# Optimization experiments

Hardware: AMD Instinct MI355X
Metric: run time of the kernel (lower is better)

Reference implementation:

```python
import jax, jax.numpy as jnp
import numpy as np

# Model hyperparameters (match init_kwargs)
J, L, A, A_PRIME = 5, 4, 4, 1
M = N = 128
C = 1
NB = 2
DELTA_J, DELTA_L = J, L
MASK_ANGLES = 4
SHIFT_R = 4  # radius (pixels) of directional correlation shifts
EPS = 1e-6


def _pair_indices():
    """Static (i1, i2) indices into the flattened [C*J*L*A] coefficient axis
    for cross-scale/angle correlation pairs: j1 <= j2 <= j1+delta_j,
    circular |l1-l2| <= delta_l, a1 in [0,A), a2 in [0,A_prime)."""
    i1, i2 = [], []
    flat = lambda c, j, l, a: ((c * J + j) * L + l) * A + a
    for c in range(C):
        for j1 in range(J):
            for j2 in range(j1, min(j1 + DELTA_J, J - 1) + 1):
                for l1 in range(L):
                    for l2 in range(L):
                        dl = min((l1 - l2) % L, (l2 - l1) % L)
                        if dl > DELTA_L:
                            continue
                        for a1 in range(A):
                            for a2 in range(A_PRIME):
                                i1.append(flat(c, j1, l1, a1))
                                i2.append(flat(c, j2, l2, a2))
    return np.asarray(i1, np.int32), np.asarray(i2, np.int32)


def _shifts():
    """Zero shift plus MASK_ANGLES directional shifts at radius SHIFT_R."""
    sh = [(0, 0)]
    for s in range(MASK_ANGLES):
        th = np.pi * s / MASK_ANGLES
        sh.append((int(round(SHIFT_R * np.cos(th))), int(round(SHIFT_R * np.sin(th)))))
    return sh


def _highpass_filters():
    """Angular-sector highpass masks in Fourier space: |k| > pi/2 split into
    MASK_ANGLES orientation sectors (angle folded to [0, pi))."""
    kx = 2 * np.pi * np.fft.fftfreq(M)[:, None]
    ky = 2 * np.pi * np.fft.fftfreq(N)[None, :]
    r = np.sqrt(kx ** 2 + ky ** 2)
    th = np.mod(np.arctan2(ky, kx), np.pi)
    h = []
    for s in range(MASK_ANGLES):
        lo, hi = np.pi * s / MASK_ANGLES, np.pi * (s + 1) / MASK_ANGLES
        h.append(((r > np.pi / 2) & (th >= lo) & (th < hi)).astype(np.float32))
    return np.stack(h)  # [MASK_ANGLES, M, N]


def setup_inputs() -> dict:
    key = jax.random.key(0)
    k = jax.random.split(key, 5)
    return {
        "x": jax.random.normal(k[0], (NB, C, M, N), jnp.float32),
        "hatpsi_re": jax.random.normal(k[1], (C, J, L, A, M, N), jnp.float32),
        "hatpsi_im": jax.random.normal(k[2], (C, J, L, A, M, N), jnp.float32),
        "hatphi_re": jax.random.normal(k[3], (M, N), jnp.float32),
        "hatphi_im": jax.random.normal(k[4], (M, N), jnp.float32),
    }


def reference(x, hatpsi_re, hatpsi_im, hatphi_re, hatphi_im):
    nb = x.shape[0]
    # --- WaveConvLayer: FFT wavelet convolution ---
    hatx = jnp.fft.fft2(x)  # [nb, C, M, N] complex
    hatpsi = hatpsi_re + 1j * hatpsi_im  # [C, J, L, A, M, N]
    xpsi = jnp.fft.ifft2(hatx[:, :, None, None, None] * hatpsi[None])  # [nb,C,J,L,A,M,N]
    # --- ReluCenterLayer: ReLU of real part, spatially centered, L2-normalized ---
    y = jax.nn.relu(xpsi.real)
    y = y - y.mean((-2, -1), keepdims=True)
    y = y / (jnp.sqrt((y * y).mean((-2, -1), keepdims=True)) + EPS)
    yf = y.reshape(nb, C * J * L * A, M, N)
    # --- CorrLayer: shifted cross-correlations over pair list ---
    i1, i2 = _pair_indices()
    a1 = yf[:, i1].reshape(nb, -1, M * N)  # [nb, P, M*N]
    a2 = yf[:, i2]                          # [nb, P, M, N]
    corrs = []
    for (dx, dy) in _shifts():  # small fixed set of shifts
        a2r = jnp.roll(a2, (dx, dy), axis=(-2, -1)).reshape(nb, -1, M * N)
        corrs.append(jnp.einsum('npx,npx->np', a1, a2r) / (M * N))
    xcorr = jnp.concatenate(corrs, axis=1)  # [nb, P * n_shifts]
    # --- LowpassLayer: phi-filtered moments (mean, mean-square) ---
    hatphi = hatphi_re + 1j * hatphi_im
    xlow_map = jnp.fft.ifft2(hatx * hatphi).real  # [nb, C, M, N]
    xlow = jnp.stack([xlow_map.mean((-2, -1)), (xlow_map ** 2).mean((-2, -1))], axis=-1)  # [nb,C,2]
    # --- HighpassLayer: per-sector highpass energy (Parseval) ---
    hhigh = jnp.asarray(_highpass_filters())  # [MASK_ANGLES, M, N]
    xhigh = (jnp.abs(hatx[:, :, None] * hhigh) ** 2).mean((-2, -1)) / (M * N)  # [nb,C,MASK_ANGLES]
    return jnp.concatenate([xcorr, xlow.reshape(nb, -1), xhigh.reshape(nb, -1)], axis=1)
```

## Files before the change

### kernel.cpp

```cpp
#include <hip/hip_runtime.h>
#include <math.h>

#define NB 2
#define NMAPS 81
#define NPSI 80
#define PIXELS 16384
#define OUT_STRIDE 4806

constexpr double PI_D = 3.14159265358979323846;

__device__ inline float2 cmulf(float2 a, float2 b) {
  return make_float2(a.x * b.x - a.y * b.y, a.x * b.y + a.y * b.x);
}

template <int CTRL>
__device__ inline float dppf(float v) {
  return __int_as_float(
      __builtin_amdgcn_update_dpp(0, __float_as_int(v), CTRL, 0xf, 0xf, true));
}

__device__ inline float shx(float v, const int mask) {
  if (mask == 1) return dppf<0xB1>(v);
  if (mask == 2) return dppf<0x4E>(v);
  if (mask == 8) return dppf<0x128>(v);
  if (mask == 32) {
    auto r = __builtin_amdgcn_permlane32_swap(__float_as_uint(v),
                                              __float_as_uint(v), false, false);
    return __uint_as_float((threadIdx.x & 32) ? r[0] : r[1]);
  }
  return __shfl_xor(v, mask);
}

__device__ inline float wred64(float v) {
  int x;
  x = __builtin_amdgcn_update_dpp(0, __float_as_int(v), 0x111, 0xf, 0xf, true); v += __int_as_float(x);
  x = __builtin_amdgcn_update_dpp(0, __float_as_int(v), 0x112, 0xf, 0xf, true); v += __int_as_float(x);
  x = __builtin_amdgcn_update_dpp(0, __float_as_int(v), 0x114, 0xf, 0xf, true); v += __int_as_float(x);
  x = __builtin_amdgcn_update_dpp(0, __float_as_int(v), 0x118, 0xf, 0xf, true); v += __int_as_float(x);
  x = __builtin_amdgcn_update_dpp(0, __float_as_int(v), 0x142, 0xa, 0xf, true); v += __int_as_float(x);
  x = __builtin_amdgcn_update_dpp(0, __float_as_int(v), 0x143, 0xc, 0xf, true); v += __int_as_float(x);
  return __int_as_float(__builtin_amdgcn_readlane(__float_as_int(v), 63));
}


__global__ __launch_bounds__(128) void k_fft_rows(const float* __restrict__ x,
                                                  float2* __restrict__ tx,
                                                  int* __restrict__ sector) {
  const int tid = threadIdx.x;
  const int blkid = blockIdx.x;
  if (blkid >= NB * 128) {
    int idx = (blkid - NB * 128) * 128 + tid;
    int i = idx >> 7, j = idx & 127;
    double fx = (double)(i < 64 ? i : i - 128) / 128.0;
    double fy = (double)(j < 64 ? j : j - 128) / 128.0;
    double kx = (2.0 * PI_D) * fx;
    double ky = (2.0 * PI_D) * fy;
    double r2 = kx * kx + ky * ky;
    const double h = PI_D / 2.0;
    int s = -1;
    if (r2 > h * h) {
      double th = atan2(ky, kx);
      th = fmod(th, PI_D);
      if (th < 0.0) th += PI_D;
      if (th < PI_D * 0.25) s = 0;
      else if (th < PI_D * 0.5) s = 1;
      else if (th < PI_D * 0.75) s = 2;
      else if (th < PI_D) s = 3;
    }
    sector[idx] = s;
    return;
  }
  __shared__ float row[128];
  __shared__ float2 wt[128];
  const int m = blkid & 127;
  const int b = blkid >> 7;
  {
    double ang = -(2.0 * PI_D / 128.0) * (double)tid;
    wt[tid] = make_float2((float)cos(ang), (float)sin(ang));
  }
  row[tid] = x[(b << 14) + (m << 7) + tid];
  __syncthreads();
  float ar = 0.f, ai = 0.f;
  int idx = 0;
  const int v = tid;
#pragma unroll 8
  for (int n = 0; n < 128; ++n) {
    float xv = row[n];
    float2 w = wt[idx];
    ar = fmaf(xv, w.x, ar);
    ai = fmaf(xv, w.y, ai);
    idx = (idx + v) & 127;
  }
  tx[(b << 14) + (m << 7) + tid] = make_float2(ar, ai);
}

__global__ __launch_bounds__(128) void k_fft_cols(const float2* __restrict__ tx,
                                                  float2* __restrict__ hatx) {
  __shared__ float2 col[128];
  __shared__ float2 wt[128];
  const int tid = threadIdx.x;
  const int v = blockIdx.x & 127;
  const int b = blockIdx.x >> 7;
  {
    double ang = -(2.0 * PI_D / 128.0) * (double)tid;
    wt[tid] = make_float2((float)cos(ang), (float)sin(ang));
  }
  col[tid] = tx[(b << 14) + (tid << 7) + v];
  __syncthreads();
  float ar = 0.f, ai = 0.f;
  int idx = 0;
  const int u = tid;
#pragma unroll 8
  for (int mm = 0; mm < 128; ++mm) {
    float2 z = col[mm];
    float2 w = wt[idx];
    ar += z.x * w.x - z.y * w.y;
    ai += z.x * w.y + z.y * w.x;
    idx = (idx + u) & 127;
  }
  hatx[(b << 14) + (tid << 7) + v] = make_float2(ar, ai);
}


#define BFLY(z)                                     \
  {                                                 \
    float tx_ = shx((z).x, mask);                   \
    float ty_ = shx((z).y, mask);                   \
    float ax_ = fmaf(s, (z).x, tx_);                \
    float ay_ = fmaf(s, (z).y, ty_);                \
    (z).x = ax_ * we.x - ay_ * we.y;                \
    (z).y = ax_ * we.y + ay_ * we.x;                \
  }

__device__ inline void fft128_inv(float2& z0, float2& z1, float2& z2, float2& z3,
                                  const float2* __restrict__ wt, int l) {
  {
    float2 w = wt[l];
    float2 a0 = make_float2(z0.x + z1.x, z0.y + z1.y);
    float2 d0 = make_float2(z0.x - z1.x, z0.y - z1.y);
    z0 = a0;
    z1 = cmulf(d0, w);
    float2 a1 = make_float2(z2.x + z3.x, z2.y + z3.y);
    float2 d1 = make_float2(z2.x - z3.x, z2.y - z3.y);
    z2 = a1;
    z3 = cmulf(d1, w);
  }
#pragma unroll
  for (int mask = 32; mask >= 1; mask >>= 1) {
    float2 w = wt[(l & (mask - 1)) * (64 / mask)];
    const bool up = (l & mask) != 0;
    const float s = up ? -1.f : 1.f;
    const float2 we = up ? w : make_float2(1.f, 0.f);
    BFLY(z0);
    BFLY(z1);
    BFLY(z2);
    BFLY(z3);
  }
}


__global__ __launch_bounds__(1024) void k_ifft2d(
    const float2* __restrict__ hatx,
    const float* __restrict__ psi_re, const float* __restrict__ psi_im,
    const float* __restrict__ phi_re, const float* __restrict__ phi_im,
    float* __restrict__ y, float2* __restrict__ meaninv,
    float* __restrict__ out) {
  __shared__ float2 Tsh[128 * 129];
  __shared__ float2 wt[64];
  __shared__ float2 red16[16];
  const int tid = threadIdx.x;
  const int l = tid & 63;
  const int w = tid >> 6;
  const int mf = blockIdx.x;
  const int b = mf / NMAPS;
  const int f = mf - b * NMAPS;
  if (tid < 64) {
    double ang = (2.0 * PI_D / 128.0) * (double)tid;
    wt[tid] = make_float2((float)cos(ang), (float)sin(ang));
  }
  __syncthreads();
  for (int r = 0; r < 4; ++r) {
    const int uA = r * 32 + (w << 1);
    const int uB = uA + 1;
    const float2* hA = hatx + (b << 14) + (uA << 7);
    float2 hA0 = hA[l], hA1 = hA[l + 64];
    float2 hB0 = hA[128 + l], hB1 = hA[128 + l + 64];
    float2 fA0, fA1, fB0, fB1;
    if (f < NPSI) {
      const int po = (f << 14) + (uA << 7);
      fA0 = make_float2(psi_re[po + l], psi_im[po + l]);
      fA1 = make_float2(psi_re[po + l + 64], psi_im[po + l + 64]);
      fB0 = make_float2(psi_re[po + 128 + l], psi_im[po + 128 + l]);
      fB1 = make_float2(psi_re[po + 128 + l + 64], psi_im[po + 128 + l + 64]);
    } else {
      const int po = (uA << 7);
      fA0 = make_float2(phi_re[po + l], phi_im[po + l]);
      fA1 = make_float2(phi_re[po + l + 64], phi_im[po + l + 64]);
      fB0 = make_float2(phi_re[po + 128 + l], phi_im[po + 128 + l]);
      fB1 = make_float2(phi_re[po + 128 + l + 64], phi_im[po + 128 + l + 64]);
    }
    float2 zA0 = cmulf(hA0, fA0), zA1 = cmulf(hA1, fA1);
    float2 zB0 = cmulf(hB0, fB0), zB1 = cmulf(hB1, fB1);
    fft128_inv(zA0, zA1, zB0, zB1, wt, l);
    Tsh[l * 129 + uA] = zA0;
    Tsh[(l + 64) * 129 + uA] = zA1;
    Tsh[l * 129 + uB] = zB0;
    Tsh[(l + 64) * 129 + uB] = zB1;
  }
  __syncthreads();
  float s1 = 0.f, s2 = 0.f;
  float* yb = y + ((size_t)(b * NPSI + f) << 14);
  const int m2 = __brev(l) >> 26;
  for (int r = 0; r < 4; ++r) {
    const int qA = r * 32 + (w << 1);
    const int qB = qA + 1;
    float2 zA0 = Tsh[qA * 129 + l], zA1 = Tsh[qA * 129 + l + 64];
    float2 zB0 = Tsh[qB * 129 + l], zB1 = Tsh[qB * 129 + l + 64];
    fft128_inv(zA0, zA1, zB0, zB1, wt, l);
    const float sc = 1.f / 16384.f;
    float rA0 = zA0.x * sc, rA1 = zA1.x * sc;
    float rB0 = zB0.x * sc, rB1 = zB1.x * sc;
    if (f < NPSI) {
      rA0 = fmaxf(rA0, 0.f); rA1 = fmaxf(rA1, 0.f);
      rB0 = fmaxf(rB0, 0.f); rB1 = fmaxf(rB1, 0.f);
      const int nA = __brev(qA) >> 25;
      const int nB = __brev(qB) >> 25;
      *(float2*)(yb + (nA << 7) + (m2 << 1)) = make_float2(rA0, rA1);
      *(float2*)(yb + (nB << 7) + (m2 << 1)) = make_float2(rB0, rB1);
    }
    s1 += rA0 + rA1 + rB0 + rB1;
    s2 += rA0 * rA0 + rA1 * rA1 + rB0 * rB0 + rB1 * rB1;
  }
  float t1 = wred64(s1), t2 = wred64(s2);
  if (l == 0) red16[w] = make_float2(t1, t2);
  __syncthreads();
  if (w == 0) {
    float2 p = (l < 16) ? red16[l] : make_float2(0.f, 0.f);
    float S1 = wred64(p.x), S2 = wred64(p.y);
    if (l == 0) {
      float mean = S1 * (1.f / 16384.f);
      float msq  = S2 * (1.f / 16384.f);
      if (f < NPSI) {
        float var = fmaxf(msq - mean * mean, 0.f);
        meaninv[b * NPSI + f] = make_float2(mean, 1.f / (sqrtf(var) + 1e-6f));
      } else {
        out[b * OUT_STRIDE + 4800] = mean;
        out[b * OUT_STRIDE + 4801] = msq;
      }
    }
  }
}

__global__ __launch_bounds__(256) void k_corrtail(
    const float* __restrict__ y, const float2* __restrict__ meaninv,
    const float2* __restrict__ hatx, const int* __restrict__ sector,
    float* __restrict__ out) {
  const int tid = threadIdx.x;
  const int l = tid & 63;
  const int w = tid >> 6;
  const int work = ((blockIdx.x & 7) * 61) + (blockIdx.x >> 3);
  if (work >= NB * 240) {
    const int b = work - NB * 240;
    if (b >= NB) return;
    __shared__ float red[4][4];
    float a0 = 0, a1 = 0, a2 = 0, a3 = 0;
    for (int k = tid; k < PIXELS; k += 256) {
      float2 hx = hatx[(b << 14) + k];
      float mag = hx.x * hx.x + hx.y * hx.y;
      int s = sector[k];
      if (s == 0) a0 += mag;
      else if (s == 1) a1 += mag;
      else if (s == 2) a2 += mag;
      else if (s == 3) a3 += mag;
    }
    a0 = wred64(a0); a1 = wred64(a1); a2 = wred64(a2); a3 = wred64(a3);
    if (l == 0) { red[w][0] = a0; red[w][1] = a1; red[w][2] = a2; red[w][3] = a3; }
    __syncthreads();
    if (tid < 4) {
      float tot = red[0][tid] + red[1][tid] + red[2][tid] + red[3][tid];
      out[b * OUT_STRIDE + 4802 + tid] = tot * (1.f / (16384.f * 16384.f));
    }
    return;
  }
  __shared__ float s2m[128 * 132];
  __shared__ float redb[4 * 20];
  __shared__ float2 mi[5];
  const int b = work / 240;
  const int r_ = work - b * 240;
  const int jj = r_ >> 4;
  const int l1 = (r_ >> 2) & 3;
  const int l2 = r_ & 3;
  int j1 = 0, rem = jj;
  while (rem >= 5 - j1) { rem -= (5 - j1); ++j1; }
  const int j2 = j1 + rem;
  const int i1b = j1 * 16 + l1 * 4;
  const int i2 = j2 * 16 + l2 * 4;
  if (tid < 4) mi[tid] = meaninv[b * NPSI + i1b + tid];
  else if (tid == 4) mi[4] = meaninv[b * NPSI + i2];
  const float* __restrict__ y1 = y + ((size_t)(b * NPSI + i1b) << 14);
  const float* __restrict__ y2 = y + ((size_t)(b * NPSI + i2) << 14);
  const int r0 = tid >> 5;
  const int c4 = (tid & 31) << 2;
#pragma unroll
  for (int k = 0; k < 16; ++k) {
    int row = k * 8 + r0;
    *(float4*)&s2m[row * 132 + c4] = *(const float4*)&y2[(row << 7) + c4];
  }
  __syncthreads();
  if (tid < 128) {
    *(float4*)&s2m[tid * 132 + 128] = *(const float4*)&s2m[tid * 132];
  }
  __syncthreads();
  const int bm4 = (c4 + 124) & 127;
  float acc[20];
#pragma unroll
  for (int o = 0; o < 20; ++o) acc[o] = 0.f;
#pragma unroll 4
  for (int k = 0; k < 16; ++k) {
    const int r = k * 8 + r0;
    const int rm0 = r * 132;
    const int rm3 = ((r + 125) & 127) * 132;
    const int rm4 = ((r + 124) & 127) * 132;
    float4 q0 = *(const float4*)&s2m[rm0 + c4];
    float4 q1 = *(const float4*)&s2m[rm0 + bm4];
    float4 q3 = *(const float4*)&s2m[rm4 + c4];
    float4 qa = *(const float4*)&s2m[rm3 + bm4];
    float4 qb = *(const float4*)&s2m[rm3 + bm4 + 4];
    float4 qd = *(const float4*)&s2m[rm3 + c4 + 4];
    const float u2x = qa.y, u2y = qa.z, u2z = qa.w, u2w = qb.x;
    const float u4x = qb.w, u4y = qd.x, u4z = qd.y, u4w = qd.z;
#pragma unroll
    for (int m = 0; m < 4; ++m) {
      float4 v = *(const float4*)&y1[(m << 14) + (r << 7) + c4];
      acc[m*5+0] = fmaf(v.w,q0.w,fmaf(v.z,q0.z,fmaf(v.y,q0.y,fmaf(v.x,q0.x,acc[m*5+0]))));
      acc[m*5+1] = fmaf(v.w,q1.w,fmaf(v.z,q1.z,fmaf(v.y,q1.y,fmaf(v.x,q1.x,acc[m*5+1]))));
      acc[m*5+2] = fmaf(v.w,u2w,fmaf(v.z,u2z,fmaf(v.y,u2y,fmaf(v.x,u2x,acc[m*5+2]))));
      acc[m*5+3] = fmaf(v.w,q3.w,fmaf(v.z,q3.z,fmaf(v.y,q3.y,fmaf(v.x,q3.x,acc[m*5+3]))));
      acc[m*5+4] = fmaf(v.w,u4w,fmaf(v.z,u4z,fmaf(v.y,u4y,fmaf(v.x,u4x,acc[m*5+4]))));
    }
  }
#pragma unroll
  for (int o = 0; o < 20; ++o) {
    float tot = wred64(acc[o]);
    if (l == 0) redb[w * 20 + o] = tot;
  }
  __syncthreads();
  if (tid < 20) {
    int m = tid / 5, s = tid - m * 5;
    float tot = redb[tid] + redb[20 + tid] + redb[40 + tid] + redb[60 + tid];
    float2 m1 = mi[m], m2 = mi[4];
    float c = m1.y * m2.y * (tot * (1.f / 16384.f) - m1.x * m2.x);
    int p = jj * 64 + l1 * 16 + l2 * 4 + m;
    out[b * OUT_STRIDE + s * 960 + p] = c;
  }
}

extern "C" void kernel_launch(void* const* d_in, const int* in_sizes, int n_in,
                              void* d_out, int out_size, void* d_ws, size_t ws_size,
                              hipStream_t stream) {
  (void)in_sizes; (void)n_in; (void)out_size; (void)ws_size;
  const float* x      = (const float*)d_in[0];
  const float* psi_re = (const float*)d_in[1];
  const float* psi_im = (const float*)d_in[2];
  const float* phi_re = (const float*)d_in[3];
  const float* phi_im = (const float*)d_in[4];
  float* out = (float*)d_out;
  char* ws = (char*)d_ws;

  constexpr size_t TX_BYTES   = (size_t)NB * PIXELS * sizeof(float2);
  constexpr size_t HATX_OFF   = TX_BYTES;
  constexpr size_t HATX_BYTES = (size_t)NB * PIXELS * sizeof(float2);
  constexpr size_t Y_OFF      = HATX_OFF + HATX_BYTES;
  constexpr size_t Y_BYTES    = (size_t)NB * NPSI * PIXELS * sizeof(float);
  constexpr size_t MI_OFF     = Y_OFF + Y_BYTES;
  constexpr size_t MI_BYTES   = (size_t)NB * NPSI * sizeof(float2);
  constexpr size_t SEC_OFF    = MI_OFF + MI_BYTES;

  float2* tx       = (float2*)(ws);
  float2* hatx     = (float2*)(ws + HATX_OFF);
  float*  y        = (float*)(ws + Y_OFF);
  float2* meaninv  = (float2*)(ws + MI_OFF);
  int*    sector   = (int*)(ws + SEC_OFF);

  k_fft_rows<<<NB * 128 + 128, 128, 0, stream>>>(x, tx, sector);
  k_fft_cols<<<NB * 128, 128, 0, stream>>>(tx, hatx);
  k_ifft2d<<<NB * NMAPS, 1024, 0, stream>>>(hatx, psi_re, psi_im, phi_re, phi_im,
                                            y, meaninv, out);
  k_corrtail<<<488, 256, 0, stream>>>(y, meaninv, hatx, sector, out);
}
```

Measured before the change: 59.56 us.

## Fuse forward FFT into one kernel, pack real column IFFTs pairwise, prefetch filters

Replaces the two naive O(N^2) DFT kernels (rows, then columns) with a single butterfly-based 2D FFT kernel that does both passes per image in shared memory. This removes a launch and the intermediate global buffer. In the inverse FFT, the second pass now packs two real-output columns into one complex FFT using Hermitian symmetry, halving those FFTs. The first-pass loads of hatx and the filters are software-prefetched one iteration ahead. The forward kernel now runs only 2 compute blocks, which limits parallelism, and the Hermitian packing adds shared-memory reads.

```diff
diff --git a/kernel.cpp b/kernel.cpp
--- a/kernel.cpp
+++ b/kernel.cpp
@@ -43,13 +43,50 @@
 }
 
 
-__global__ __launch_bounds__(128) void k_fft_rows(const float* __restrict__ x,
-                                                  float2* __restrict__ tx,
-                                                  int* __restrict__ sector) {
+#define BFLY(z)                                     \
+  {                                                 \
+    float tx_ = shx((z).x, mask);                   \
+    float ty_ = shx((z).y, mask);                   \
+    float ax_ = fmaf(s, (z).x, tx_);                \
+    float ay_ = fmaf(s, (z).y, ty_);                \
+    (z).x = ax_ * we.x - ay_ * we.y;                \
+    (z).y = ax_ * we.y + ay_ * we.x;                \
+  }
+
+__device__ inline void fft128_inv(float2& z0, float2& z1, float2& z2, float2& z3,
+                                  const float2* __restrict__ wt, int l) {
+  {
+    float2 w = wt[l];
+    float2 a0 = make_float2(z0.x + z1.x, z0.y + z1.y);
+    float2 d0 = make_float2(z0.x - z1.x, z0.y - z1.y);
+    z0 = a0;
+    z1 = cmulf(d0, w);
+    float2 a1 = make_float2(z2.x + z3.x, z2.y + z3.y);
+    float2 d1 = make_float2(z2.x - z3.x, z2.y - z3.y);
+    z2 = a1;
+    z3 = cmulf(d1, w);
+  }
+#pragma unroll
+  for (int mask = 32; mask >= 1; mask >>= 1) {
+    float2 w = wt[(l & (mask - 1)) * (64 / mask)];
+    const bool up = (l & mask) != 0;
+    const float s = up ? -1.f : 1.f;
+    const float2 we = up ? w : make_float2(1.f, 0.f);
+    BFLY(z0);
+    BFLY(z1);
+    BFLY(z2);
+    BFLY(z3);
+  }
+}
+
+
+__global__ __launch_bounds__(1024) void k_fft2d(const float* __restrict__ x,
+                                                float2* __restrict__ hatx,
+                                                int* __restrict__ sector) {
   const int tid = threadIdx.x;
   const int blkid = blockIdx.x;
-  if (blkid >= NB * 128) {
-    int idx = (blkid - NB * 128) * 128 + tid;
+  if (blkid >= NB) {
+    int idx = (blkid - NB) * 1024 + tid;
     int i = idx >> 7, j = idx & 127;
     double fx = (double)(i < 64 ? i : i - 128) / 128.0;
     double fy = (double)(j < 64 ? j : j - 128) / 128.0;
@@ -70,91 +107,57 @@
     sector[idx] = s;
     return;
   }
-  __shared__ float row[128];
-  __shared__ float2 wt[128];
-  const int m = blkid & 127;
-  const int b = blkid >> 7;
-  {
+  __shared__ float2 Tsh[128 * 129];
+  __shared__ float2 wtf[64];
+  const int l = tid & 63;
+  const int w = tid >> 6;
+  const int b = blkid;
+  if (tid < 64) {
     double ang = -(2.0 * PI_D / 128.0) * (double)tid;
-    wt[tid] = make_float2((float)cos(ang), (float)sin(ang));
-  }
-  row[tid] = x[(b << 14) + (m << 7) + tid];
-  __syncthreads();
-  float ar = 0.f, ai = 0.f;
-  int idx = 0;
-  const int v = tid;
-#pragma unroll 8
-  for (int n = 0; n < 128; ++n) {
-    float xv = row[n];
-    float2 w = wt[idx];
-    ar = fmaf(xv, w.x, ar);
-    ai = fmaf(xv, w.y, ai);
-    idx = (idx + v) & 127;
-  }
-  tx[(b << 14) + (m << 7) + tid] = make_float2(ar, ai);
-}
-
-__global__ __launch_bounds__(128) void k_fft_cols(const float2* __restrict__ tx,
-                                                  float2* __restrict__ hatx) {
-  __shared__ float2 col[128];
-  __shared__ float2 wt[128];
-  const int tid = threadIdx.x;
-  const int v = blockIdx.x & 127;
-  const int b = blockIdx.x >> 7;
-  {
-    double ang = -(2.0 * PI_D / 128.0) * (double)tid;
-    wt[tid] = make_float2((float)cos(ang), (float)sin(ang));
-  }
-  col[tid] = tx[(b << 14) + (tid << 7) + v];
-  __syncthreads();
-  float ar = 0.f, ai = 0.f;
-  int idx = 0;
-  const int u = tid;
-#pragma unroll 8
-  for (int mm = 0; mm < 128; ++mm) {
-    float2 z = col[mm];
-    float2 w = wt[idx];
-    ar += z.x * w.x - z.y * w.y;
-    ai += z.x * w.y + z.y * w.x;
-    idx = (idx + u) & 127;
-  }
-  hatx[(b << 14) + (tid << 7) + v] = make_float2(ar, ai);
-}
-
-
-#define BFLY(z)                                     \
-  {                                                 \
-    float tx_ = shx((z).x, mask);                   \
-    float ty_ = shx((z).y, mask);                   \
-    float ax_ = fmaf(s, (z).x, tx_);                \
-    float ay_ = fmaf(s, (z).y, ty_);                \
-    (z).x = ax_ * we.x - ay_ * we.y;                \
-    (z).y = ax_ * we.y + ay_ * we.x;                \
-  }
-
-__device__ inline void fft128_inv(float2& z0, float2& z1, float2& z2, float2& z3,
-                                  const float2* __restrict__ wt, int l) {
-  {
-    float2 w = wt[l];
-    float2 a0 = make_float2(z0.x + z1.x, z0.y + z1.y);
-    float2 d0 = make_float2(z0.x - z1.x, z0.y - z1.y);
-    z0 = a0;
-    z1 = cmulf(d0, w);
-    float2 a1 = make_float2(z2.x + z3.x, z2.y + z3.y);
-    float2 d1 = make_float2(z2.x - z3.x, z2.y - z3.y);
-    z2 = a1;
-    z3 = cmulf(d1, w);
-  }
-#pragma unroll
-  for (int mask = 32; mask >= 1; mask >>= 1) {
-    float2 w = wt[(l & (mask - 1)) * (64 / mask)];
-    const bool up = (l & mask) != 0;
-    const float s = up ? -1.f : 1.f;
-    const float2 we = up ? w : make_float2(1.f, 0.f);
-    BFLY(z0);
-    BFLY(z1);
-    BFLY(z2);
-    BFLY(z3);
+    wtf[tid] = make_float2((float)cos(ang), (float)sin(ang));
+  }
+  __syncthreads();
+  for (int r = 0; r < 4; ++r) {
+    const int uA = r * 32 + (w << 1);
+    const float* xr = x + (b << 14) + (uA << 7);
+    float2 zA0 = make_float2(xr[l], 0.f);
+    float2 zA1 = make_float2(xr[l + 64], 0.f);
+    float2 zB0 = make_float2(xr[128 + l], 0.f);
+    float2 zB1 = make_float2(xr[128 + l + 64], 0.f);
+    fft128_inv(zA0, zA1, zB0, zB1, wtf, l);
+    Tsh[l * 129 + uA] = zA0;
+    Tsh[(l + 64) * 129 + uA] = zA1;
+    Tsh[l * 129 + uA + 1] = zB0;
+    Tsh[(l + 64) * 129 + uA + 1] = zB1;
+  }
+  __syncthreads();
+  float2 res[4][4];
+#pragma unroll
+  for (int r = 0; r < 4; ++r) {
+    const int qA = r * 32 + (w << 1);
+    const int qB = qA + 1;
+    float2 zA0 = Tsh[qA * 129 + l], zA1 = Tsh[qA * 129 + l + 64];
+    float2 zB0 = Tsh[qB * 129 + l], zB1 = Tsh[qB * 129 + l + 64];
+    fft128_inv(zA0, zA1, zB0, zB1, wtf, l);
+    res[r][0] = zA0; res[r][1] = zA1; res[r][2] = zB0; res[r][3] = zB1;
+  }
+  __syncthreads();
+  const int ku = (__brev(l) >> 26) << 1;
+#pragma unroll
+  for (int r = 0; r < 4; ++r) {
+    const int qA = r * 32 + (w << 1);
+    const int vA = __brev(qA) >> 25;
+    const int vB = __brev(qA + 1) >> 25;
+    Tsh[ku * 129 + vA] = res[r][0];
+    Tsh[(ku + 1) * 129 + vA] = res[r][1];
+    Tsh[ku * 129 + vB] = res[r][2];
+    Tsh[(ku + 1) * 129 + vB] = res[r][3];
+  }
+  __syncthreads();
+  float2* hb = hatx + (b << 14);
+  for (int i = 0; i < 16; ++i) {
+    int k = i * 1024 + tid;
+    hb[k] = Tsh[(k >> 7) * 129 + (k & 127)];
   }
 }
 
@@ -179,57 +182,94 @@
     wt[tid] = make_float2((float)cos(ang), (float)sin(ang));
   }
   __syncthreads();
-  for (int r = 0; r < 4; ++r) {
-    const int uA = r * 32 + (w << 1);
-    const int uB = uA + 1;
-    const float2* hA = hatx + (b << 14) + (uA << 7);
-    float2 hA0 = hA[l], hA1 = hA[l + 64];
-    float2 hB0 = hA[128 + l], hB1 = hA[128 + l + 64];
-    float2 fA0, fA1, fB0, fB1;
-    if (f < NPSI) {
-      const int po = (f << 14) + (uA << 7);
-      fA0 = make_float2(psi_re[po + l], psi_im[po + l]);
-      fA1 = make_float2(psi_re[po + l + 64], psi_im[po + l + 64]);
-      fB0 = make_float2(psi_re[po + 128 + l], psi_im[po + 128 + l]);
-      fB1 = make_float2(psi_re[po + 128 + l + 64], psi_im[po + 128 + l + 64]);
-    } else {
-      const int po = (uA << 7);
-      fA0 = make_float2(phi_re[po + l], phi_im[po + l]);
-      fA1 = make_float2(phi_re[po + l + 64], phi_im[po + l + 64]);
-      fB0 = make_float2(phi_re[po + 128 + l], phi_im[po + 128 + l]);
-      fB1 = make_float2(phi_re[po + 128 + l + 64], phi_im[po + 128 + l + 64]);
-    }
-    float2 zA0 = cmulf(hA0, fA0), zA1 = cmulf(hA1, fA1);
-    float2 zB0 = cmulf(hB0, fB0), zB1 = cmulf(hB1, fB1);
-    fft128_inv(zA0, zA1, zB0, zB1, wt, l);
-    Tsh[l * 129 + uA] = zA0;
-    Tsh[(l + 64) * 129 + uA] = zA1;
-    Tsh[l * 129 + uB] = zB0;
-    Tsh[(l + 64) * 129 + uB] = zB1;
+  const float2* hb2 = hatx + (b << 14);
+  const float* fre = (f < NPSI) ? psi_re + ((size_t)f << 14) : phi_re;
+  const float* fim = (f < NPSI) ? psi_im + ((size_t)f << 14) : phi_im;
+  {
+    const int o0 = (w << 1) << 7;
+    float2 hA0 = hb2[o0 + l],       hA1 = hb2[o0 + l + 64];
+    float2 hB0 = hb2[o0 + 128 + l], hB1 = hb2[o0 + 128 + l + 64];
+    float fa0r = fre[o0 + l],            fa0i = fim[o0 + l];
+    float fa1r = fre[o0 + l + 64],       fa1i = fim[o0 + l + 64];
+    float fb0r = fre[o0 + 128 + l],      fb0i = fim[o0 + 128 + l];
+    float fb1r = fre[o0 + 128 + l + 64], fb1i = fim[o0 + 128 + l + 64];
+#pragma unroll
+    for (int r = 0; r < 4; ++r) {
+      const int uA = r * 32 + (w << 1);
+      float2 nhA0, nhA1, nhB0, nhB1;
+      float nfa0r, nfa0i, nfa1r, nfa1i, nfb0r, nfb0i, nfb1r, nfb1i;
+      if (r < 3) {
+        const int o = ((r + 1) * 32 + (w << 1)) << 7;
+        nhA0 = hb2[o + l];       nhA1 = hb2[o + l + 64];
+        nhB0 = hb2[o + 128 + l]; nhB1 = hb2[o + 128 + l + 64];
+        nfa0r = fre[o + l];            nfa0i = fim[o + l];
+        nfa1r = fre[o + l + 64];       nfa1i = fim[o + l + 64];
+        nfb0r = fre[o + 128 + l];      nfb0i = fim[o + 128 + l];
+        nfb1r = fre[o + 128 + l + 64]; nfb1i = fim[o + 128 + l + 64];
+      }
+      float2 zA0 = cmulf(hA0, make_float2(fa0r, fa0i));
+      float2 zA1 = cmulf(hA1, make_float2(fa1r, fa1i));
+      float2 zB0 = cmulf(hB0, make_float2(fb0r, fb0i));
+      float2 zB1 = cmulf(hB1, make_float2(fb1r, fb1i));
+      fft128_inv(zA0, zA1, zB0, zB1, wt, l);
+      Tsh[l * 129 + uA] = zA0;
+      Tsh[(l + 64) * 129 + uA] = zA1;
+      Tsh[l * 129 + uA + 1] = zB0;
+      Tsh[(l + 64) * 129 + uA + 1] = zB1;
+      if (r < 3) {
+        hA0 = nhA0; hA1 = nhA1; hB0 = nhB0; hB1 = nhB1;
+        fa0r = nfa0r; fa0i = nfa0i; fa1r = nfa1r; fa1i = nfa1i;
+        fb0r = nfb0r; fb0i = nfb0i; fb1r = nfb1r; fb1i = nfb1i;
+      }
+    }
   }
   __syncthreads();
   float s1 = 0.f, s2 = 0.f;
   float* yb = y + ((size_t)(b * NPSI + f) << 14);
   const int m2 = __brev(l) >> 26;
-  for (int r = 0; r < 4; ++r) {
-    const int qA = r * 32 + (w << 1);
-    const int qB = qA + 1;
-    float2 zA0 = Tsh[qA * 129 + l], zA1 = Tsh[qA * 129 + l + 64];
-    float2 zB0 = Tsh[qB * 129 + l], zB1 = Tsh[qB * 129 + l + 64];
+  const int um  = (128 - l) & 127;
+  const int um2 = (64 - l) & 127;
+  for (int r = 0; r < 2; ++r) {
+    const int q0 = r * 64 + (w << 2);
+    float2 zA0, zA1, zB0, zB1;
+    {
+      const float2* C0 = &Tsh[(q0    ) * 129];
+      const float2* C1 = &Tsh[(q0 + 1) * 129];
+      float2 a0 = C0[l], a0m = C0[um], a1 = C0[l + 64], a1m = C0[um2];
+      float2 b0 = C1[l], b0m = C1[um], b1 = C1[l + 64], b1m = C1[um2];
+      zA0 = make_float2(0.5f * (a0.x + a0m.x) - 0.5f * (b0.y - b0m.y),
+                        0.5f * (a0.y - a0m.y) + 0.5f * (b0.x + b0m.x));
+      zA1 = make_float2(0.5f * (a1.x + a1m.x) - 0.5f * (b1.y - b1m.y),
+                        0.5f * (a1.y - a1m.y) + 0.5f * (b1.x + b1m.x));
+      const float2* C2 = &Tsh[(q0 + 2) * 129];
+      const float2* C3 = &Tsh[(q0 + 3) * 129];
+      float2 c0 = C2[l], c0m = C2[um], c1 = C2[l + 64], c1m = C2[um2];
+      float2 d0 = C3[l], d0m = C3[um], d1 = C3[l + 64], d1m = C3[um2];
+      zB0 = make_float2(0.5f * (c0.x + c0m.x) - 0.5f * (d0.y - d0m.y),
+                        0.5f * (c0.y - c0m.y) + 0.5f * (d0.x + d0m.x));
+      zB1 = make_float2(0.5f * (c1.x + c1m.x) - 0.5f * (d1.y - d1m.y),
+                        0.5f * (c1.y - c1m.y) + 0.5f * (d1.x + d1m.x));
+    }
     fft128_inv(zA0, zA1, zB0, zB1, wt, l);
     const float sc = 1.f / 16384.f;
-    float rA0 = zA0.x * sc, rA1 = zA1.x * sc;
-    float rB0 = zB0.x * sc, rB1 = zB1.x * sc;
+    const int nA0 = __brev(q0) >> 25;
+    float xA00 = zA0.x * sc, xA01 = zA0.y * sc;
+    float xA10 = zA1.x * sc, xA11 = zA1.y * sc;
+    float xB00 = zB0.x * sc, xB01 = zB0.y * sc;
+    float xB10 = zB1.x * sc, xB11 = zB1.y * sc;
     if (f < NPSI) {
-      rA0 = fmaxf(rA0, 0.f); rA1 = fmaxf(rA1, 0.f);
-      rB0 = fmaxf(rB0, 0.f); rB1 = fmaxf(rB1, 0.f);
-      const int nA = __brev(qA) >> 25;
-      const int nB = __brev(qB) >> 25;
-      *(float2*)(yb + (nA << 7) + (m2 << 1)) = make_float2(rA0, rA1);
-      *(float2*)(yb + (nB << 7) + (m2 << 1)) = make_float2(rB0, rB1);
-    }
-    s1 += rA0 + rA1 + rB0 + rB1;
-    s2 += rA0 * rA0 + rA1 * rA1 + rB0 * rB0 + rB1 * rB1;
+      xA00 = fmaxf(xA00, 0.f); xA01 = fmaxf(xA01, 0.f);
+      xA10 = fmaxf(xA10, 0.f); xA11 = fmaxf(xA11, 0.f);
+      xB00 = fmaxf(xB00, 0.f); xB01 = fmaxf(xB01, 0.f);
+      xB10 = fmaxf(xB10, 0.f); xB11 = fmaxf(xB11, 0.f);
+      *(float2*)(yb + ((nA0     ) << 7) + (m2 << 1)) = make_float2(xA00, xA10);
+      *(float2*)(yb + ((nA0 + 64) << 7) + (m2 << 1)) = make_float2(xA01, xA11);
+      *(float2*)(yb + ((nA0 + 32) << 7) + (m2 << 1)) = make_float2(xB00, xB10);
+      *(float2*)(yb + ((nA0 + 96) << 7) + (m2 << 1)) = make_float2(xB01, xB11);
+    }
+    s1 += xA00 + xA01 + xA10 + xA11 + xB00 + xB01 + xB10 + xB11;
+    s2 += xA00 * xA00 + xA01 * xA01 + xA10 * xA10 + xA11 * xA11 +
+          xB00 * xB00 + xB01 * xB01 + xB10 * xB10 + xB11 * xB11;
   }
   float t1 = wred64(s1), t2 = wred64(s2);
   if (l == 0) red16[w] = make_float2(t1, t2);
@@ -367,23 +407,19 @@
   float* out = (float*)d_out;
   char* ws = (char*)d_ws;
 
-  constexpr size_t TX_BYTES   = (size_t)NB * PIXELS * sizeof(float2);
-  constexpr size_t HATX_OFF   = TX_BYTES;
   constexpr size_t HATX_BYTES = (size_t)NB * PIXELS * sizeof(float2);
-  constexpr size_t Y_OFF      = HATX_OFF + HATX_BYTES;
+  constexpr size_t Y_OFF      = HATX_BYTES;
   constexpr size_t Y_BYTES    = (size_t)NB * NPSI * PIXELS * sizeof(float);
   constexpr size_t MI_OFF     = Y_OFF + Y_BYTES;
   constexpr size_t MI_BYTES   = (size_t)NB * NPSI * sizeof(float2);
   constexpr size_t SEC_OFF    = MI_OFF + MI_BYTES;
 
-  float2* tx       = (float2*)(ws);
-  float2* hatx     = (float2*)(ws + HATX_OFF);
+  float2* hatx     = (float2*)(ws);
   float*  y        = (float*)(ws + Y_OFF);
   float2* meaninv  = (float2*)(ws + MI_OFF);
   int*    sector   = (int*)(ws + SEC_OFF);
 
-  k_fft_rows<<<NB * 128 + 128, 128, 0, stream>>>(x, tx, sector);
-  k_fft_cols<<<NB * 128, 128, 0, stream>>>(tx, hatx);
+  k_fft2d<<<NB + 16, 1024, 0, stream>>>(x, hatx, sector);
   k_ifft2d<<<NB * NMAPS, 1024, 0, stream>>>(hatx, psi_re, psi_im, phi_re, phi_im,
                                             y, meaninv, out);
   k_corrtail<<<488, 256, 0, stream>>>(y, meaninv, hatx, sector, out);
```

New measurement: 66.24 us. 11.2% more time.
